# Kernel optimization log

Measured on AMD Instinct MI355X. Metric: run time of the kernel, lower is better.

Reference implementation:

```python
import jax, jax.numpy as jnp
import numpy as np

N, E, HN, K = 4096, 8192, 1024, 8
NF, EF = 128, 64
NH = [256, 256]
EH = [64, 64]
EMB = NH[-1] + len(EH)  # 258
BN_EPS = 1e-5


def setup_inputs() -> dict:
    key = jax.random.key(0)
    ks = jax.random.split(key, 16)

    def nrm(k, shape, fan):
        return jax.random.normal(k, shape, jnp.float32) / np.float32(np.sqrt(fan))

    return {
        "X_n": jax.random.normal(ks[0], (N, NF), jnp.float32),
        "X_e": jax.random.normal(ks[1], (E, EF), jnp.float32),
        # row-normalized-ish adjacency and scaled Laplacian to keep activations bounded
        "A_tilde": jax.random.uniform(ks[2], (N, N), jnp.float32) / np.float32(N),
        "L1_tilde": jax.random.normal(ks[3], (E, E), jnp.float32) / np.float32(np.sqrt(E)),
        "B1": jax.random.normal(ks[4], (N, E), jnp.float32) / np.float32(np.sqrt(E)),
        # GNN params (Linear stores weight as [out, in])
        "gnn_W1": nrm(ks[5], (NH[0], NF), NF), "gnn_b1": jnp.zeros((NH[0],), jnp.float32),
        "gnn_W2": nrm(ks[6], (NH[1], NH[0]), NH[0]), "gnn_b2": jnp.zeros((NH[1],), jnp.float32),
        # HoSC layer 1: in=EF, out=EH[0]
        "hosc_W1": nrm(ks[7], (EH[0], EF), EF), "hosc_b1": jnp.zeros((EH[0],), jnp.float32),
        "bn1_g": jnp.ones((EH[0],), jnp.float32), "bn1_b": jnp.zeros((EH[0],), jnp.float32),
        # HoSC layer 2: in=1 (after channel-max), out=EH[1]
        "hosc_W2": nrm(ks[8], (EH[1], 1), 1), "hosc_b2": jnp.zeros((EH[1],), jnp.float32),
        "bn2_g": jnp.ones((EH[1],), jnp.float32), "bn2_b": jnp.zeros((EH[1],), jnp.float32),
        # heads
        "node_W": nrm(ks[9], (1, EMB), EMB), "node_b": jnp.zeros((1,), jnp.float32),
        "edge_W": nrm(ks[10], (1, len(EH)), len(EH)), "edge_b": jnp.zeros((1,), jnp.float32),
        "hyper_W": nrm(ks[11], (1, EMB), EMB), "hyper_b": jnp.zeros((1,), jnp.float32),
        "hyperedges": jax.random.randint(ks[12], (HN, K), 0, N, jnp.int64),
    }


def _bn(x, g, b):
    # training-mode BatchNorm1d: biased batch statistics over rows
    m = jnp.mean(x, axis=0)
    v = jnp.var(x, axis=0)
    return g * (x - m) / jnp.sqrt(v + BN_EPS) + b


def _hosc_layer(Z, L1, W, bias, g, b):
    Zt = Z @ W.T + bias            # [E, out]
    Zc = L1 @ Zt                   # [E, out]
    Zp = jax.nn.relu(_bn(Zc, g, b))
    return jnp.max(Zp, axis=1, keepdims=True)  # [E, 1]


def reference(X_n, X_e, A_tilde, L1_tilde, B1,
              gnn_W1, gnn_b1, gnn_W2, gnn_b2,
              hosc_W1, hosc_b1, bn1_g, bn1_b,
              hosc_W2, hosc_b2, bn2_g, bn2_b,
              node_W, node_b, edge_W, edge_b, hyper_W, hyper_b,
              hyperedges):
    # --- GNN over nodes ---
    H = jax.nn.relu((A_tilde @ X_n) @ gnn_W1.T + gnn_b1)   # [N, 256]
    H_n = jax.nn.relu((A_tilde @ H) @ gnn_W2.T + gnn_b2)   # [N, 256]

    # --- HoSC over edges ---
    Z1 = _hosc_layer(X_e, L1_tilde, hosc_W1, hosc_b1, bn1_g, bn1_b)  # [E, 1]
    Z2 = _hosc_layer(Z1, L1_tilde, hosc_W2, hosc_b2, bn2_g, bn2_b)   # [E, 1]
    Z_H = jnp.concatenate([Z1, Z2], axis=1)                 # [E, 2]

    # --- fuse edge info into nodes ---
    H_e = B1 @ Z_H                                          # [N, 2]
    Hcat = jnp.concatenate([H_n, H_e], axis=1)              # [N, 258]

    node_prob = jax.nn.sigmoid(Hcat @ node_W.T + node_b).squeeze(-1)  # [N]
    edge_prob = jax.nn.sigmoid(Z_H @ edge_W.T + edge_b).squeeze(-1)   # [E]

    # vectorized hyperedge gather-mean-linear-sigmoid (fixed-size hyperedges)
    hfeat = Hcat[hyperedges].mean(axis=1)                   # [HN, 258]
    hyperedge_prob = jax.nn.sigmoid(hfeat @ hyper_W.T + hyper_b)  # [HN, 1]

    return node_prob, edge_prob, hyperedge_prob, Hcat
```

## Files before the change

### kernel.cpp

```cpp
#include <hip/hip_runtime.h>
#include <hip/hip_bf16.h>

using f32x4  = __attribute__((ext_vector_type(4))) float;
using u32x4  = __attribute__((ext_vector_type(4))) unsigned int;
using bf16x8 = __attribute__((ext_vector_type(8))) short;

__device__ __forceinline__ ushort f2bf(float x) {
    union { __hip_bfloat16 h; ushort u; } cv;
    cv.h = __float2bfloat16(x);
    return cv.u;
}
__device__ __forceinline__ unsigned pk2(float lo, float hi) {
    return (unsigned)f2bf(lo) | ((unsigned)f2bf(hi) << 16);
}
__device__ __forceinline__ float sigmoidf_(float x) { return 1.f / (1.f + expf(-x)); }

template<int NSUM, bool A_BF16, bool ABR, bool SPLIT, bool RELU, bool BF16_OUT, bool HAS_BIAS>
__device__ __forceinline__ void gemm_body(
    ushort* As, ushort* Bs,
    const void* __restrict__ Avoid, const ushort* __restrict__ B,
    const float* __restrict__ abias, const float* __restrict__ bias,
    float* __restrict__ Cf, ushort* __restrict__ Cb,
    int M, int N, int K, int ldc, int kPerChunk, long pStride,
    int bx, int by, int bz)
{
    const int tid  = threadIdx.x;
    const int lane = tid & 63;
    const int wid  = tid >> 6;
    const int wr   = wid >> 1, wc = wid & 1;
    const int g    = lane >> 4, lr = lane & 15;
    const long m0  = (long)bx * 128;
    const int  n0  = by * 64;

    int kbeg = 0, kend = K;
    if (SPLIT) { kbeg = bz * kPerChunk; kend = kbeg + kPerChunk; if (kend > K) kend = K; }

    const int bkr = tid & 31;
    const int bcb = tid >> 5;

    const float*  Af = (const float*)Avoid;
    const ushort* Ab = (const ushort*)Avoid;

    f32x4 pa[4];
    u32x4 pab[2];
    u32x4 pb;

    auto loadT = [&](int k0) {
        if (A_BF16) {
#pragma unroll
            for (int i = 0; i < 2; i++) {
                int s = tid + 256 * i; int row = s >> 2, c8 = s & 3;
                pab[i] = *(const u32x4*)(Ab + (m0 + row) * (long)K + k0 + c8 * 8);
            }
        } else {
#pragma unroll
            for (int i = 0; i < 4; i++) {
                int s = tid + 256 * i; int row = s >> 3, c4 = s & 7;
                const float* base = Af + (m0 + row) * (long)K + k0 + c4 * 4;
                f32x4 v = *(const f32x4*)base;
                if (NSUM > 0) {
#pragma unroll
                    for (int z = 1; z < NSUM; z++) v += *(const f32x4*)(base + z * pStride);
                }
                if (ABR) {
                    f32x4 bq = *(const f32x4*)(abias + k0 + c4 * 4);
                    v.x = fmaxf(v.x + bq.x, 0.f);
                    v.y = fmaxf(v.y + bq.y, 0.f);
                    v.z = fmaxf(v.z + bq.z, 0.f);
                    v.w = fmaxf(v.w + bq.w, 0.f);
                }
                pa[i] = v;
            }
        }
        pb = *(const u32x4*)(B + (long)(k0 + bkr) * N + n0 + bcb * 8);
    };
    auto storeT = [&]() {
        if (A_BF16) {
#pragma unroll
            for (int i = 0; i < 2; i++) {
                int s = tid + 256 * i; int row = s >> 2, c8 = s & 3;
                *(u32x4*)(&As[row * 40 + c8 * 8]) = pab[i];
            }
        } else {
#pragma unroll
            for (int i = 0; i < 4; i++) {
                int s = tid + 256 * i; int row = s >> 3, c4 = s & 7;
                ushort4 w;
                w.x = f2bf(pa[i].x); w.y = f2bf(pa[i].y);
                w.z = f2bf(pa[i].z); w.w = f2bf(pa[i].w);
                *(ushort4*)(&As[row * 40 + c4 * 4]) = w;
            }
        }
        const ushort* p8 = (const ushort*)&pb;
#pragma unroll
        for (int j = 0; j < 8; j++) Bs[(bcb * 8 + j) * 40 + bkr] = p8[j];
    };

    f32x4 acc[4][2] = {};

    const int nk = (kend - kbeg) >> 5;
    loadT(kbeg);
    for (int t = 0; t < nk; ++t) {
        storeT();
        __syncthreads();
        if (t + 1 < nk) loadT(kbeg + ((t + 1) << 5));
        bf16x8 af[4], bfr[2];
#pragma unroll
        for (int fm = 0; fm < 4; fm++)
            af[fm] = *(const bf16x8*)(&As[(wr * 64 + fm * 16 + lr) * 40 + g * 8]);
#pragma unroll
        for (int fn = 0; fn < 2; fn++)
            bfr[fn] = *(const bf16x8*)(&Bs[(wc * 32 + fn * 16 + lr) * 40 + g * 8]);
#pragma unroll
        for (int fm = 0; fm < 4; fm++)
#pragma unroll
            for (int fn = 0; fn < 2; fn++)
                acc[fm][fn] = __builtin_amdgcn_mfma_f32_16x16x32_bf16(af[fm], bfr[fn], acc[fm][fn], 0, 0, 0);
        __syncthreads();
    }

    if (SPLIT) {
        float* P = Cf + (long)bz * M * N;
#pragma unroll
        for (int fm = 0; fm < 4; fm++)
#pragma unroll
            for (int fn = 0; fn < 2; fn++)
#pragma unroll
                for (int rr = 0; rr < 4; rr++) {
                    long row = m0 + wr * 64 + fm * 16 + g * 4 + rr;
                    int  col = n0 + wc * 32 + fn * 16 + lr;
                    P[row * N + col] = acc[fm][fn][rr];
                }
    } else {
#pragma unroll
        for (int fm = 0; fm < 4; fm++)
#pragma unroll
            for (int fn = 0; fn < 2; fn++)
#pragma unroll
                for (int rr = 0; rr < 4; rr++) {
                    long row = m0 + wr * 64 + fm * 16 + g * 4 + rr;
                    int  col = n0 + wc * 32 + fn * 16 + lr;
                    float v = acc[fm][fn][rr];
                    if (HAS_BIAS) v += bias[col];
                    if (RELU) v = fmaxf(v, 0.f);
                    if (BF16_OUT) Cb[row * ldc + col] = f2bf(v);
                    else          Cf[row * ldc + col] = v;
                }
    }
}

__global__ __launch_bounds__(256)
void prep_k(const float* __restrict__ A, ushort* __restrict__ Abf,
            const float* __restrict__ Xn, const float* __restrict__ W1, ushort* __restrict__ T1,
            const float* __restrict__ Xe, const float* __restrict__ Wh,
            const float* __restrict__ hb, ushort* __restrict__ Zt1,
            const float* __restrict__ W2, ushort* __restrict__ W2t,
            float* __restrict__ stats)
{
    __shared__ float xs[1024];
    int b = blockIdx.x, t = threadIdx.x;
    if (b < 8192) {
        long j = (long)b * 256 + t;
        f32x4 v0 = ((const f32x4*)A)[2 * j];
        f32x4 v1 = ((const f32x4*)A)[2 * j + 1];
        u32x4 w;
        w.x = pk2(v0.x, v0.y); w.y = pk2(v0.z, v0.w);
        w.z = pk2(v1.x, v1.y); w.w = pk2(v1.z, v1.w);
        ((u32x4*)Abf)[j] = w;
    } else if (b < 8704) {
        int r0 = (b - 8192) * 8;
        for (int idx = t; idx < 1024; idx += 256) xs[idx] = Xn[(long)r0 * 128 + idx];
        __syncthreads();
        float acc[8] = {};
        const float* wrow = W1 + (long)t * 128;
        for (int i = 0; i < 128; i++) {
            float w = wrow[i];
#pragma unroll
            for (int r = 0; r < 8; r++) acc[r] += xs[r * 128 + i] * w;
        }
#pragma unroll
        for (int r = 0; r < 8; r++) T1[(long)(r0 + r) * 256 + t] = f2bf(acc[r]);
    } else if (b < 10752) {
        int row = (b - 8704) * 4 + (t >> 6);
        int o   = t & 63;
        const float* xr = Xe + (long)row * 64;
        const float* wr = Wh + (long)o * 64;
        float acc = hb[o];
#pragma unroll 8
        for (int i = 0; i < 64; i++) acc += xr[i] * wr[i];
        Zt1[(long)row * 64 + o] = f2bf(acc);
    } else if (b < 11008) {
        int j = (b - 10752) * 256 + t;
        int i = j >> 8, o = j & 255;
        W2t[j] = f2bf(W2[o * 256 + i]);
    } else {
        if (t < 256) stats[t] = 0.f;
    }
}

__device__ __forceinline__ void bnred_body(int b, const float* __restrict__ P,
                                           float* __restrict__ Zc,
                                           float* __restrict__ gsum, float* __restrict__ gsq)
{
    const long MN = 8192 * 64;
    int t = threadIdx.x;
    int c = t & 63, rg = t >> 6;
    float sx = 0.f, sq = 0.f;
    int base = b * 32 + rg;
#pragma unroll 4
    for (int i = 0; i < 8; i++) {
        long idx = (long)(base + 4 * i) * 64 + c;
        float x = 0.f;
#pragma unroll
        for (int z = 0; z < 8; z++) x += P[idx + z * MN];
        Zc[idx] = x;
        sx += x; sq += x * x;
    }
    __shared__ float ls[256], lq[256];
    ls[t] = sx; lq[t] = sq;
    __syncthreads();
    if (t < 64) {
        float a = ls[t] + ls[t + 64] + ls[t + 128] + ls[t + 192];
        float q = lq[t] + lq[t + 64] + lq[t + 128] + lq[t + 192];
        atomicAdd(&gsum[t], a);
        atomicAdd(&gsq[t], q);
    }
}

__device__ __forceinline__ void z1_body(int b, const float* __restrict__ Zc,
                                        const float* __restrict__ gsum, const float* __restrict__ gsq,
                                        const float* __restrict__ g, const float* __restrict__ bb,
                                        float* __restrict__ Z1)
{
    int w = threadIdx.x >> 6, lane = threadIdx.x & 63;
    int row = b * 4 + w;
    const float inv = 1.f / 8192.f;
    float m = gsum[lane] * inv;
    float v = gsq[lane] * inv - m * m;
    float x = Zc[row * 64 + lane];
    float y = fmaxf(g[lane] * (x - m) * rsqrtf(v + 1e-5f) + bb[lane], 0.f);
#pragma unroll
    for (int o = 32; o > 0; o >>= 1) y = fmaxf(y, __shfl_xor(y, o));
    if (lane == 0) Z1[row] = y;
}

__device__ __forceinline__ void pass2_body(int row, const float* __restrict__ L1,
                                           const float* __restrict__ Z1,
                                           float* __restrict__ s, float* __restrict__ r)
{
    int t = threadIdx.x;
    int l = t & 63, w = t >> 6;
    const f32x4* rp = (const f32x4*)(L1 + (long)row * 8192);
    const f32x4* z4 = (const f32x4*)Z1;
    float as = 0.f, ar = 0.f;
#pragma unroll 4
    for (int k = 0; k < 8; k++) {
        f32x4 v = rp[t + 256 * k];
        f32x4 z = z4[t + 256 * k];
        as += v.x * z.x + v.y * z.y + v.z * z.z + v.w * z.w;
        ar += v.x + v.y + v.z + v.w;
    }
#pragma unroll
    for (int o = 32; o > 0; o >>= 1) { as += __shfl_xor(as, o); ar += __shfl_xor(ar, o); }
    __shared__ float sw[4], rw[4];
    if (l == 0) { sw[w] = as; rw[w] = ar; }
    __syncthreads();
    if (t == 0) {
        s[row] = sw[0] + sw[1] + sw[2] + sw[3];
        r[row] = rw[0] + rw[1] + rw[2] + rw[3];
    }
}

__device__ __forceinline__ void hcatred_body(int b, const float* __restrict__ P2,
                                             const float* __restrict__ b2, float* __restrict__ hcat)
{
    const long MNq = (long)4096 * 256 / 4;
    int j = b * 256 + threadIdx.x;
    int row = j >> 6, c4 = (j & 63) * 4;
    const f32x4* Q = (const f32x4*)P2;
    f32x4 v = Q[j] + Q[j + MNq] + Q[j + 2 * MNq] + Q[j + 3 * MNq];
    f32x4 bq = *(const f32x4*)(b2 + c4);
    float* dst = hcat + (long)row * 258 + c4;
    float2 lo = { fmaxf(v.x + bq.x, 0.f), fmaxf(v.y + bq.y, 0.f) };
    float2 hi = { fmaxf(v.z + bq.z, 0.f), fmaxf(v.w + bq.w, 0.f) };
    *(float2*)dst = lo;
    *(float2*)(dst + 2) = hi;
}

__global__ __launch_bounds__(256)
void dual_a_k(const float* __restrict__ L1, const ushort* __restrict__ Zt1, float* __restrict__ Pa,
              const ushort* __restrict__ Abf, const ushort* __restrict__ T1, float* __restrict__ Pb)
{
    __shared__ ushort As[128 * 40];
    __shared__ ushort Bs[64 * 40];
    int bid = blockIdx.x;
    if (bid < 512) {
        gemm_body<0, false, false, true, false, false, false>(
            As, Bs, L1, Zt1, nullptr, nullptr, Pa, nullptr,
            8192, 64, 8192, 64, 1024, 0, bid & 63, 0, bid >> 6);
    } else {
        int b = bid - 512;
        gemm_body<0, true, false, true, false, false, false>(
            As, Bs, Abf, T1, nullptr, nullptr, Pb, nullptr,
            4096, 256, 4096, 256, 1024, 0, b & 31, (b >> 5) & 3, b >> 7);
    }
}

__global__ __launch_bounds__(256)
void dual_b_k(const float* __restrict__ Pb, const float* __restrict__ gb1,
              const ushort* __restrict__ W2t, ushort* __restrict__ T2,
              const float* __restrict__ Pa, float* __restrict__ Zc1,
              float* __restrict__ gsum, float* __restrict__ gsq)
{
    __shared__ ushort As[128 * 40];
    __shared__ ushort Bs[64 * 40];
    int bid = blockIdx.x;
    if (bid < 128) {
        gemm_body<4, false, true, false, false, true, false>(
            As, Bs, Pb, W2t, gb1, nullptr, nullptr, T2,
            4096, 256, 256, 256, 0, (long)4096 * 256, bid & 31, bid >> 5, 0);
    } else {
        bnred_body(bid - 128, Pa, Zc1, gsum, gsq);
    }
}

__global__ __launch_bounds__(256)
void dual_c_k(const ushort* __restrict__ Abf, const ushort* __restrict__ T2, float* __restrict__ Pa,
              const float* __restrict__ Zc1, const float* __restrict__ gsum,
              const float* __restrict__ gsq, const float* __restrict__ bn1g,
              const float* __restrict__ bn1b, float* __restrict__ Z1)
{
    __shared__ ushort As[128 * 40];
    __shared__ ushort Bs[64 * 40];
    int bid = blockIdx.x;
    if (bid < 512) {
        gemm_body<0, true, false, true, false, false, false>(
            As, Bs, Abf, T2, nullptr, nullptr, Pa, nullptr,
            4096, 256, 4096, 256, 1024, 0, bid & 31, (bid >> 5) & 3, bid >> 7);
    } else {
        z1_body(bid - 512, Zc1, gsum, gsq, bn1g, bn1b, Z1);
    }
}

__global__ __launch_bounds__(256)
void dual_d_k(const float* __restrict__ Pa, const float* __restrict__ gb2, float* __restrict__ hcat,
              const float* __restrict__ L1, const float* __restrict__ Z1,
              float* __restrict__ s, float* __restrict__ r)
{
    int bid = blockIdx.x;
    if (bid < 1024) hcatred_body(bid, Pa, gb2, hcat);
    else            pass2_body(bid - 1024, L1, Z1, s, r);
}

__global__ __launch_bounds__(1024) void stats2_k(const float* __restrict__ s, const float* __restrict__ r,
                                                 float* __restrict__ S5)
{
    int t = threadIdx.x, l = t & 63, w = t >> 6;
    float Ss = 0, Sr = 0, Sss = 0, Srr = 0, Ssr = 0;
    for (int i = t; i < 8192; i += 1024) {
        float sv = s[i], rv = r[i];
        Ss += sv; Sr += rv; Sss += sv * sv; Srr += rv * rv; Ssr += sv * rv;
    }
#pragma unroll
    for (int o = 32; o > 0; o >>= 1) {
        Ss += __shfl_xor(Ss, o); Sr += __shfl_xor(Sr, o);
        Sss += __shfl_xor(Sss, o); Srr += __shfl_xor(Srr, o); Ssr += __shfl_xor(Ssr, o);
    }
    __shared__ float buf[16][5];
    if (l == 0) { buf[w][0] = Ss; buf[w][1] = Sr; buf[w][2] = Sss; buf[w][3] = Srr; buf[w][4] = Ssr; }
    __syncthreads();
    if (t < 5) {
        float a = 0.f;
#pragma unroll
        for (int i = 0; i < 16; i++) a += buf[i][t];
        S5[t] = a;
    }
}

__global__ __launch_bounds__(256) void z2_edge_k(const float* __restrict__ s, const float* __restrict__ r,
                                                 const float* __restrict__ S,
                                                 const float* __restrict__ W2, const float* __restrict__ b2,
                                                 const float* __restrict__ g2, const float* __restrict__ bb2,
                                                 const float* __restrict__ eW, const float* __restrict__ eb,
                                                 const float* __restrict__ Z1,
                                                 float* __restrict__ Z2, float* __restrict__ edge_out)
{
    int w = threadIdx.x >> 6, lane = threadIdx.x & 63;
    int row = blockIdx.x * 4 + w;
    const float inv = 1.f / 8192.f;
    float ms = S[0] * inv, mr = S[1] * inv;
    float vs = S[2] * inv - ms * ms;
    float vr = S[3] * inv - mr * mr;
    float cv = S[4] * inv - ms * mr;
    float w2 = W2[lane], bz = b2[lane];
    float mc = w2 * ms + bz * mr;
    float vc = w2 * w2 * vs + 2.f * w2 * bz * cv + bz * bz * vr;
    float x  = w2 * s[row] + bz * r[row];
    float y  = fmaxf(g2[lane] * (x - mc) * rsqrtf(vc + 1e-5f) + bb2[lane], 0.f);
#pragma unroll
    for (int o = 32; o > 0; o >>= 1) y = fmaxf(y, __shfl_xor(y, o));
    if (lane == 0) {
        Z2[row] = y;
        float e = Z1[row] * eW[0] + y * eW[1] + eb[0];
        edge_out[row] = sigmoidf_(e);
    }
}

__global__ __launch_bounds__(256) void he_node_k(const float* __restrict__ B1, const float* __restrict__ Z1,
                                                 const float* __restrict__ Z2, float* __restrict__ hcat,
                                                 const float* __restrict__ nW, const float* __restrict__ nb,
                                                 float* __restrict__ node_out)
{
    int n = blockIdx.x, t = threadIdx.x;
    int l = t & 63, w = t >> 6;
    const f32x4* rp  = (const f32x4*)(B1 + (long)n * 8192);
    const f32x4* z1v = (const f32x4*)Z1;
    const f32x4* z2v = (const f32x4*)Z2;
    float a1 = 0.f, a2 = 0.f;
#pragma unroll 4
    for (int k = 0; k < 8; k++) {
        f32x4 v = rp[t + 256 * k];
        f32x4 p = z1v[t + 256 * k];
        f32x4 q = z2v[t + 256 * k];
        a1 += v.x * p.x + v.y * p.y + v.z * p.z + v.w * p.w;
        a2 += v.x * q.x + v.y * q.y + v.z * q.z + v.w * q.w;
    }
    float d = hcat[(long)n * 258 + t] * nW[t];
#pragma unroll
    for (int o = 32; o > 0; o >>= 1) {
        a1 += __shfl_xor(a1, o); a2 += __shfl_xor(a2, o); d += __shfl_xor(d, o);
    }
    __shared__ float s1[4], s2[4], s3[4];
    if (l == 0) { s1[w] = a1; s2[w] = a2; s3[w] = d; }
    __syncthreads();
    if (t == 0) {
        float A1 = s1[0] + s1[1] + s1[2] + s1[3];
        float A2 = s2[0] + s2[1] + s2[2] + s2[3];
        float D  = s3[0] + s3[1] + s3[2] + s3[3];
        hcat[(long)n * 258 + 256] = A1;
        hcat[(long)n * 258 + 257] = A2;
        node_out[n] = sigmoidf_(D + A1 * nW[256] + A2 * nW[257] + nb[0]);
    }
}

__global__ __launch_bounds__(256) void hyper_k(const void* __restrict__ he_idx,
                                               const float* __restrict__ hcat,
                                               const float* __restrict__ hW, const float* __restrict__ hb,
                                               float* __restrict__ out)
{
    int w = threadIdx.x >> 6, lane = threadIdx.x & 63;
    int h = blockIdx.x * 4 + w;
    const unsigned int* u = (const unsigned int*)he_idx;
    unsigned int odd = u[2 * lane + 1];
    bool is64 = __all(odd == 0u);
    float acc = 0.f;
    for (int k = 0; k < 8; k++) {
        int idx;
        if (is64) idx = (int)((const long long*)he_idx)[h * 8 + k];
        else      idx = ((const int*)he_idx)[h * 8 + k];
        const float* hr = hcat + (long)idx * 258;
        for (int d = lane; d < 258; d += 64) acc += hr[d] * hW[d];
    }
    acc *= 0.125f;
#pragma unroll
    for (int o = 32; o > 0; o >>= 1) acc += __shfl_xor(acc, o);
    if (lane == 0) out[h] = sigmoidf_(acc + hb[0]);
}

extern "C" void kernel_launch(void* const* d_in, const int* in_sizes, int n_in,
                              void* d_out, int out_size, void* d_ws, size_t ws_size,
                              hipStream_t stream)
{
    const float* X_n  = (const float*)d_in[0];
    const float* X_e  = (const float*)d_in[1];
    const float* A_t  = (const float*)d_in[2];
    const float* L1   = (const float*)d_in[3];
    const float* B1   = (const float*)d_in[4];
    const float* gW1  = (const float*)d_in[5];
    const float* gb1  = (const float*)d_in[6];
    const float* gW2  = (const float*)d_in[7];
    const float* gb2  = (const float*)d_in[8];
    const float* hW1  = (const float*)d_in[9];
    const float* hb1  = (const float*)d_in[10];
    const float* bn1g = (const float*)d_in[11];
    const float* bn1b = (const float*)d_in[12];
    const float* hW2  = (const float*)d_in[13];
    const float* hb2  = (const float*)d_in[14];
    const float* bn2g = (const float*)d_in[15];
    const float* bn2b = (const float*)d_in[16];
    const float* nW   = (const float*)d_in[17];
    const float* nb   = (const float*)d_in[18];
    const float* eW   = (const float*)d_in[19];
    const float* ebb  = (const float*)d_in[20];
    const float* yW   = (const float*)d_in[21];
    const float* yb   = (const float*)d_in[22];
    const void*  he   = d_in[23];

    float* out       = (float*)d_out;
    float* out_node  = out;
    float* out_edge  = out + 4096;
    float* out_hyper = out + 12288;
    float* hcat      = out + 13312;

    size_t off = 0;
    auto alloc = [&](size_t bytes) {
        void* p = (char*)d_ws + off;
        off = (off + bytes + 255) & ~(size_t)255;
        return p;
    };
    ushort* Abf   = (ushort*)alloc((size_t)4096 * 4096 * 2);
    ushort* T1    = (ushort*)alloc(4096 * 256 * 2);
    ushort* T2    = (ushort*)alloc(4096 * 256 * 2);
    ushort* Zt1   = (ushort*)alloc(8192 * 64 * 2);
    ushort* W2t   = (ushort*)alloc(256 * 256 * 2);
    float*  Zc1   = (float*)alloc(8192 * 64 * 4);
    float*  stats = (float*)alloc(256 * 4);
    float*  gsum  = stats;
    float*  gsq   = stats + 64;
    float*  S5    = stats + 128;
    float*  Z1    = (float*)alloc(8192 * 4);
    float*  Z2    = (float*)alloc(8192 * 4);
    float*  sbuf  = (float*)alloc(8192 * 4);
    float*  rbuf  = (float*)alloc(8192 * 4);
    float*  Pa    = (float*)alloc((size_t)8192 * 64 * 8 * 4);
    float*  Pb    = (float*)alloc((size_t)4096 * 256 * 4 * 4);

    prep_k<<<11009, 256, 0, stream>>>(A_t, Abf, X_n, gW1, T1, X_e, hW1, hb1, Zt1,
                                      gW2, W2t, stats);

    dual_a_k<<<1024, 256, 0, stream>>>(L1, Zt1, Pa, Abf, T1, Pb);

    dual_b_k<<<384, 256, 0, stream>>>(Pb, gb1, W2t, T2, Pa, Zc1, gsum, gsq);

    dual_c_k<<<2560, 256, 0, stream>>>(Abf, T2, Pa, Zc1, gsum, gsq, bn1g, bn1b, Z1);

    dual_d_k<<<9216, 256, 0, stream>>>(Pa, gb2, hcat, L1, Z1, sbuf, rbuf);

    stats2_k<<<1, 1024, 0, stream>>>(sbuf, rbuf, S5);

    z2_edge_k<<<2048, 256, 0, stream>>>(sbuf, rbuf, S5, hW2, hb2, bn2g, bn2b,
                                        eW, ebb, Z1, Z2, out_edge);

    he_node_k<<<4096, 256, 0, stream>>>(B1, Z1, Z2, hcat, nW, nb, out_node);

    hyper_k<<<256, 256, 0, stream>>>(he, hcat, yW, yb, out_hyper);
}
```

Before: 291.6 us.

## Deepen split-K partitions, replace BN atomics with last-block reduction, fold stats kernel

Raises split-K depth for the L1 GEMM from 8 to 32 chunks and for the A_tilde GEMMs from 4 to 8, so many more blocks run in the first and third stages. The reduction kernels are widened to sum the extra partials. BN1 statistics now go into per-block partial buffers and are finished by the last-arriving block through a counter, instead of atomics on shared accumulators. The separate single-block stats2 kernel is removed, and each z2_edge block recomputes the global s/r statistics itself. In exchange, much more partial-sum traffic goes through memory and every z2 block rereads the full s/r arrays.

```diff
diff --git a/kernel.cpp b/kernel.cpp
--- a/kernel.cpp
+++ b/kernel.cpp
@@ -200,30 +200,53 @@
 
 __device__ __forceinline__ void bnred_body(int b, const float* __restrict__ P,
                                            float* __restrict__ Zc,
-                                           float* __restrict__ gsum, float* __restrict__ gsq)
-{
-    const long MN = 8192 * 64;
+                                           float* __restrict__ pstats,
+                                           float* __restrict__ gsum, float* __restrict__ gsq,
+                                           unsigned* __restrict__ ctr)
+{
+    const long MNq = (long)8192 * 64 / 4;
     int t = threadIdx.x;
-    int c = t & 63, rg = t >> 6;
-    float sx = 0.f, sq = 0.f;
-    int base = b * 32 + rg;
-#pragma unroll 4
-    for (int i = 0; i < 8; i++) {
-        long idx = (long)(base + 4 * i) * 64 + c;
-        float x = 0.f;
-#pragma unroll
-        for (int z = 0; z < 8; z++) x += P[idx + z * MN];
-        Zc[idx] = x;
-        sx += x; sq += x * x;
-    }
-    __shared__ float ls[256], lq[256];
-    ls[t] = sx; lq[t] = sq;
+    f32x4 sx = {0.f, 0.f, 0.f, 0.f};
+    f32x4 sq = {0.f, 0.f, 0.f, 0.f};
+    const f32x4* Q = (const f32x4*)P;
+#pragma unroll
+    for (int it = 0; it < 2; it++) {
+        long q = (long)b * 512 + it * 256 + t;
+        f32x4 x = {0.f, 0.f, 0.f, 0.f};
+#pragma unroll 8
+        for (int z = 0; z < 32; z++) x += Q[q + z * MNq];
+        ((f32x4*)Zc)[q] = x;
+        sx += x;
+        sq.x += x.x * x.x; sq.y += x.y * x.y; sq.z += x.z * x.z; sq.w += x.w * x.w;
+    }
+    __shared__ float ls[256][8];
+#pragma unroll
+    for (int j = 0; j < 4; j++) { ls[t][j] = sx[j]; ls[t][4 + j] = sq[j]; }
     __syncthreads();
     if (t < 64) {
-        float a = ls[t] + ls[t + 64] + ls[t + 128] + ls[t + 192];
-        float q = lq[t] + lq[t + 64] + lq[t + 128] + lq[t + 192];
-        atomicAdd(&gsum[t], a);
-        atomicAdd(&gsq[t], q);
+        int cg = t >> 2, j = t & 3;
+        float a = 0.f, qq = 0.f;
+#pragma unroll
+        for (int k = 0; k < 16; k++) { a += ls[cg + 16 * k][j]; qq += ls[cg + 16 * k][4 + j]; }
+        pstats[b * 128 + t]      = a;
+        pstats[b * 128 + 64 + t] = qq;
+    }
+    __threadfence();
+    __syncthreads();
+    __shared__ unsigned lastflag;
+    if (t == 0) {
+        unsigned old = atomicAdd(ctr, 1u);
+        lastflag = (old == 255u);
+    }
+    __syncthreads();
+    if (lastflag) {
+        __threadfence();
+        if (t < 128) {
+            float a = 0.f;
+            for (int bb = 0; bb < 256; bb++) a += pstats[bb * 128 + t];
+            if (t < 64) gsum[t] = a;
+            else        gsq[t - 64] = a;
+        }
     }
 }
 
@@ -271,14 +294,16 @@
     }
 }
 
-__device__ __forceinline__ void hcatred_body(int b, const float* __restrict__ P2,
+__device__ __forceinline__ void hcatred_body(int b, const float* __restrict__ P,
                                              const float* __restrict__ b2, float* __restrict__ hcat)
 {
     const long MNq = (long)4096 * 256 / 4;
     int j = b * 256 + threadIdx.x;
     int row = j >> 6, c4 = (j & 63) * 4;
-    const f32x4* Q = (const f32x4*)P2;
-    f32x4 v = Q[j] + Q[j + MNq] + Q[j + 2 * MNq] + Q[j + 3 * MNq];
+    const f32x4* Q = (const f32x4*)P;
+    f32x4 v = {0.f, 0.f, 0.f, 0.f};
+#pragma unroll
+    for (int z = 0; z < 8; z++) v += Q[j + z * MNq];
     f32x4 bq = *(const f32x4*)(b2 + c4);
     float* dst = hcat + (long)row * 258 + c4;
     float2 lo = { fmaxf(v.x + bq.x, 0.f), fmaxf(v.y + bq.y, 0.f) };
@@ -294,15 +319,15 @@
     __shared__ ushort As[128 * 40];
     __shared__ ushort Bs[64 * 40];
     int bid = blockIdx.x;
-    if (bid < 512) {
+    if (bid < 2048) {
         gemm_body<0, false, false, true, false, false, false>(
             As, Bs, L1, Zt1, nullptr, nullptr, Pa, nullptr,
-            8192, 64, 8192, 64, 1024, 0, bid & 63, 0, bid >> 6);
+            8192, 64, 8192, 64, 256, 0, bid & 63, 0, bid >> 6);
     } else {
-        int b = bid - 512;
+        int b = bid - 2048;
         gemm_body<0, true, false, true, false, false, false>(
             As, Bs, Abf, T1, nullptr, nullptr, Pb, nullptr,
-            4096, 256, 4096, 256, 1024, 0, b & 31, (b >> 5) & 3, b >> 7);
+            4096, 256, 4096, 256, 512, 0, b & 31, (b >> 5) & 3, b >> 7);
     }
 }
 
@@ -310,22 +335,23 @@
 void dual_b_k(const float* __restrict__ Pb, const float* __restrict__ gb1,
               const ushort* __restrict__ W2t, ushort* __restrict__ T2,
               const float* __restrict__ Pa, float* __restrict__ Zc1,
-              float* __restrict__ gsum, float* __restrict__ gsq)
+              float* __restrict__ pstats,
+              float* __restrict__ gsum, float* __restrict__ gsq, unsigned* __restrict__ ctr)
 {
     __shared__ ushort As[128 * 40];
     __shared__ ushort Bs[64 * 40];
     int bid = blockIdx.x;
     if (bid < 128) {
-        gemm_body<4, false, true, false, false, true, false>(
+        gemm_body<8, false, true, false, false, true, false>(
             As, Bs, Pb, W2t, gb1, nullptr, nullptr, T2,
             4096, 256, 256, 256, 0, (long)4096 * 256, bid & 31, bid >> 5, 0);
     } else {
-        bnred_body(bid - 128, Pa, Zc1, gsum, gsq);
+        bnred_body(bid - 128, Pa, Zc1, pstats, gsum, gsq, ctr);
     }
 }
 
 __global__ __launch_bounds__(256)
-void dual_c_k(const ushort* __restrict__ Abf, const ushort* __restrict__ T2, float* __restrict__ Pa,
+void dual_c_k(const ushort* __restrict__ Abf, const ushort* __restrict__ T2, float* __restrict__ Pb,
               const float* __restrict__ Zc1, const float* __restrict__ gsum,
               const float* __restrict__ gsq, const float* __restrict__ bn1g,
               const float* __restrict__ bn1b, float* __restrict__ Z1)
@@ -333,31 +359,36 @@
     __shared__ ushort As[128 * 40];
     __shared__ ushort Bs[64 * 40];
     int bid = blockIdx.x;
-    if (bid < 512) {
+    if (bid < 1024) {
         gemm_body<0, true, false, true, false, false, false>(
-            As, Bs, Abf, T2, nullptr, nullptr, Pa, nullptr,
-            4096, 256, 4096, 256, 1024, 0, bid & 31, (bid >> 5) & 3, bid >> 7);
+            As, Bs, Abf, T2, nullptr, nullptr, Pb, nullptr,
+            4096, 256, 4096, 256, 512, 0, bid & 31, (bid >> 5) & 3, bid >> 7);
     } else {
-        z1_body(bid - 512, Zc1, gsum, gsq, bn1g, bn1b, Z1);
+        z1_body(bid - 1024, Zc1, gsum, gsq, bn1g, bn1b, Z1);
     }
 }
 
 __global__ __launch_bounds__(256)
-void dual_d_k(const float* __restrict__ Pa, const float* __restrict__ gb2, float* __restrict__ hcat,
+void dual_d_k(const float* __restrict__ Pb, const float* __restrict__ gb2, float* __restrict__ hcat,
               const float* __restrict__ L1, const float* __restrict__ Z1,
               float* __restrict__ s, float* __restrict__ r)
 {
     int bid = blockIdx.x;
-    if (bid < 1024) hcatred_body(bid, Pa, gb2, hcat);
+    if (bid < 1024) hcatred_body(bid, Pb, gb2, hcat);
     else            pass2_body(bid - 1024, L1, Z1, s, r);
 }
 
-__global__ __launch_bounds__(1024) void stats2_k(const float* __restrict__ s, const float* __restrict__ r,
-                                                 float* __restrict__ S5)
+__global__ __launch_bounds__(256)
+void z2_edge_k(const float* __restrict__ s, const float* __restrict__ r,
+               const float* __restrict__ W2, const float* __restrict__ b2,
+               const float* __restrict__ g2, const float* __restrict__ bb2,
+               const float* __restrict__ eW, const float* __restrict__ eb,
+               const float* __restrict__ Z1,
+               float* __restrict__ Z2, float* __restrict__ edge_out)
 {
     int t = threadIdx.x, l = t & 63, w = t >> 6;
     float Ss = 0, Sr = 0, Sss = 0, Srr = 0, Ssr = 0;
-    for (int i = t; i < 8192; i += 1024) {
+    for (int i = t; i < 8192; i += 256) {
         float sv = s[i], rv = r[i];
         Ss += sv; Sr += rv; Sss += sv * sv; Srr += rv * rv; Ssr += sv * rv;
     }
@@ -366,40 +397,29 @@
         Ss += __shfl_xor(Ss, o); Sr += __shfl_xor(Sr, o);
         Sss += __shfl_xor(Sss, o); Srr += __shfl_xor(Srr, o); Ssr += __shfl_xor(Ssr, o);
     }
-    __shared__ float buf[16][5];
+    __shared__ float buf[4][5];
     if (l == 0) { buf[w][0] = Ss; buf[w][1] = Sr; buf[w][2] = Sss; buf[w][3] = Srr; buf[w][4] = Ssr; }
     __syncthreads();
-    if (t < 5) {
-        float a = 0.f;
-#pragma unroll
-        for (int i = 0; i < 16; i++) a += buf[i][t];
-        S5[t] = a;
-    }
-}
-
-__global__ __launch_bounds__(256) void z2_edge_k(const float* __restrict__ s, const float* __restrict__ r,
-                                                 const float* __restrict__ S,
-                                                 const float* __restrict__ W2, const float* __restrict__ b2,
-                                                 const float* __restrict__ g2, const float* __restrict__ bb2,
-                                                 const float* __restrict__ eW, const float* __restrict__ eb,
-                                                 const float* __restrict__ Z1,
-                                                 float* __restrict__ Z2, float* __restrict__ edge_out)
-{
-    int w = threadIdx.x >> 6, lane = threadIdx.x & 63;
+    float S0 = buf[0][0] + buf[1][0] + buf[2][0] + buf[3][0];
+    float S1 = buf[0][1] + buf[1][1] + buf[2][1] + buf[3][1];
+    float S2 = buf[0][2] + buf[1][2] + buf[2][2] + buf[3][2];
+    float S3 = buf[0][3] + buf[1][3] + buf[2][3] + buf[3][3];
+    float S4 = buf[0][4] + buf[1][4] + buf[2][4] + buf[3][4];
+
     int row = blockIdx.x * 4 + w;
     const float inv = 1.f / 8192.f;
-    float ms = S[0] * inv, mr = S[1] * inv;
-    float vs = S[2] * inv - ms * ms;
-    float vr = S[3] * inv - mr * mr;
-    float cv = S[4] * inv - ms * mr;
-    float w2 = W2[lane], bz = b2[lane];
+    float ms = S0 * inv, mr = S1 * inv;
+    float vs = S2 * inv - ms * ms;
+    float vr = S3 * inv - mr * mr;
+    float cv = S4 * inv - ms * mr;
+    float w2 = W2[l], bz = b2[l];
     float mc = w2 * ms + bz * mr;
     float vc = w2 * w2 * vs + 2.f * w2 * bz * cv + bz * bz * vr;
     float x  = w2 * s[row] + bz * r[row];
-    float y  = fmaxf(g2[lane] * (x - mc) * rsqrtf(vc + 1e-5f) + bb2[lane], 0.f);
+    float y  = fmaxf(g2[l] * (x - mc) * rsqrtf(vc + 1e-5f) + bb2[l], 0.f);
 #pragma unroll
     for (int o = 32; o > 0; o >>= 1) y = fmaxf(y, __shfl_xor(y, o));
-    if (lane == 0) {
+    if (l == 0) {
         Z2[row] = y;
         float e = Z1[row] * eW[0] + y * eW[1] + eb[0];
         edge_out[row] = sigmoidf_(e);
@@ -508,37 +528,36 @@
         off = (off + bytes + 255) & ~(size_t)255;
         return p;
     };
-    ushort* Abf   = (ushort*)alloc((size_t)4096 * 4096 * 2);
-    ushort* T1    = (ushort*)alloc(4096 * 256 * 2);
-    ushort* T2    = (ushort*)alloc(4096 * 256 * 2);
-    ushort* Zt1   = (ushort*)alloc(8192 * 64 * 2);
-    ushort* W2t   = (ushort*)alloc(256 * 256 * 2);
-    float*  Zc1   = (float*)alloc(8192 * 64 * 4);
-    float*  stats = (float*)alloc(256 * 4);
-    float*  gsum  = stats;
-    float*  gsq   = stats + 64;
-    float*  S5    = stats + 128;
-    float*  Z1    = (float*)alloc(8192 * 4);
-    float*  Z2    = (float*)alloc(8192 * 4);
-    float*  sbuf  = (float*)alloc(8192 * 4);
-    float*  rbuf  = (float*)alloc(8192 * 4);
-    float*  Pa    = (float*)alloc((size_t)8192 * 64 * 8 * 4);
-    float*  Pb    = (float*)alloc((size_t)4096 * 256 * 4 * 4);
+    ushort* Abf    = (ushort*)alloc((size_t)4096 * 4096 * 2);
+    ushort* T1     = (ushort*)alloc(4096 * 256 * 2);
+    ushort* T2     = (ushort*)alloc(4096 * 256 * 2);
+    ushort* Zt1    = (ushort*)alloc(8192 * 64 * 2);
+    ushort* W2t    = (ushort*)alloc(256 * 256 * 2);
+    float*  Zc1    = (float*)alloc(8192 * 64 * 4);
+    float*  stats  = (float*)alloc(256 * 4);
+    float*  gsum   = stats;
+    float*  gsq    = stats + 64;
+    unsigned* ctr  = (unsigned*)(stats + 192);
+    float*  pstats = (float*)alloc(256 * 128 * 4);
+    float*  Z1     = (float*)alloc(8192 * 4);
+    float*  Z2     = (float*)alloc(8192 * 4);
+    float*  sbuf   = (float*)alloc(8192 * 4);
+    float*  rbuf   = (float*)alloc(8192 * 4);
+    float*  Pa     = (float*)alloc((size_t)8192 * 64 * 32 * 4);
+    float*  Pb     = (float*)alloc((size_t)4096 * 256 * 8 * 4);
 
     prep_k<<<11009, 256, 0, stream>>>(A_t, Abf, X_n, gW1, T1, X_e, hW1, hb1, Zt1,
                                       gW2, W2t, stats);
 
-    dual_a_k<<<1024, 256, 0, stream>>>(L1, Zt1, Pa, Abf, T1, Pb);
-
-    dual_b_k<<<384, 256, 0, stream>>>(Pb, gb1, W2t, T2, Pa, Zc1, gsum, gsq);
-
-    dual_c_k<<<2560, 256, 0, stream>>>(Abf, T2, Pa, Zc1, gsum, gsq, bn1g, bn1b, Z1);
-
-    dual_d_k<<<9216, 256, 0, stream>>>(Pa, gb2, hcat, L1, Z1, sbuf, rbuf);
-
-    stats2_k<<<1, 1024, 0, stream>>>(sbuf, rbuf, S5);
-
-    z2_edge_k<<<2048, 256, 0, stream>>>(sbuf, rbuf, S5, hW2, hb2, bn2g, bn2b,
+    dual_a_k<<<3072, 256, 0, stream>>>(L1, Zt1, Pa, Abf, T1, Pb);
+
+    dual_b_k<<<384, 256, 0, stream>>>(Pb, gb1, W2t, T2, Pa, Zc1, pstats, gsum, gsq, ctr);
+
+    dual_c_k<<<3072, 256, 0, stream>>>(Abf, T2, Pb, Zc1, gsum, gsq, bn1g, bn1b, Z1);
+
+    dual_d_k<<<9216, 256, 0, stream>>>(Pb, gb2, hcat, L1, Z1, sbuf, rbuf);
+
+    z2_edge_k<<<2048, 256, 0, stream>>>(sbuf, rbuf, hW2, hb2, bn2g, bn2b,
                                         eW, ebb, Z1, Z2, out_edge);
 
     he_node_k<<<4096, 256, 0, stream>>>(B1, Z1, Z2, hcat, nW, nb, out_node);
```

Measured after the change: 380.4 us. +30.5%, slower.

## Store GEMM B operands transposed to vectorize shared-memory B staging

Applied to the files above, without the earlier changes.

Changes the B operand of all GEMMs to an N-major (transposed) layout, so each thread loads 8 contiguous k values and writes them to shared memory with one 16-byte store. Previously the tile was transposed through 8 scalar LDS writes per thread. Producers are updated to match: prep writes T1 and Zt1 transposed, W2 is no longer transposed, and the T2 GEMM gains a transposed bf16 epilogue. The transposed global writes in prep (strided scalar stores for Zt1T) and the new epilogue may be less coalesced. The epilogue also has a dead ReLU line.

```diff
diff --git a/kernel.cpp b/kernel.cpp
--- a/kernel.cpp
+++ b/kernel.cpp
@@ -15,10 +15,10 @@
 }
 __device__ __forceinline__ float sigmoidf_(float x) { return 1.f / (1.f + expf(-x)); }
 
-template<int NSUM, bool A_BF16, bool ABR, bool SPLIT, bool RELU, bool BF16_OUT, bool HAS_BIAS>
+template<int NSUM, bool A_BF16, bool ABR, bool SPLIT, bool RELU, bool BF16_OUT, bool CT_OUT, bool HAS_BIAS>
 __device__ __forceinline__ void gemm_body(
     ushort* As, ushort* Bs,
-    const void* __restrict__ Avoid, const ushort* __restrict__ B,
+    const void* __restrict__ Avoid, const ushort* __restrict__ BT,
     const float* __restrict__ abias, const float* __restrict__ bias,
     float* __restrict__ Cf, ushort* __restrict__ Cb,
     int M, int N, int K, int ldc, int kPerChunk, long pStride,
@@ -35,8 +35,8 @@
     int kbeg = 0, kend = K;
     if (SPLIT) { kbeg = bz * kPerChunk; kend = kbeg + kPerChunk; if (kend > K) kend = K; }
 
-    const int bkr = tid & 31;
-    const int bcb = tid >> 5;
+    const int bn = tid >> 2;
+    const int bk = (tid & 3) * 8;
 
     const float*  Af = (const float*)Avoid;
     const ushort* Ab = (const ushort*)Avoid;
@@ -72,7 +72,7 @@
                 pa[i] = v;
             }
         }
-        pb = *(const u32x4*)(B + (long)(k0 + bkr) * N + n0 + bcb * 8);
+        pb = *(const u32x4*)(BT + (long)(n0 + bn) * K + k0 + bk);
     };
     auto storeT = [&]() {
         if (A_BF16) {
@@ -91,9 +91,7 @@
                 *(ushort4*)(&As[row * 40 + c4 * 4]) = w;
             }
         }
-        const ushort* p8 = (const ushort*)&pb;
-#pragma unroll
-        for (int j = 0; j < 8; j++) Bs[(bcb * 8 + j) * 40 + bkr] = p8[j];
+        *(u32x4*)(&Bs[bn * 40 + bk]) = pb;
     };
 
     f32x4 acc[4][2] = {};
@@ -131,6 +129,21 @@
                     int  col = n0 + wc * 32 + fn * 16 + lr;
                     P[row * N + col] = acc[fm][fn][rr];
                 }
+    } else if (CT_OUT) {
+#pragma unroll
+        for (int fm = 0; fm < 4; fm++)
+#pragma unroll
+            for (int fn = 0; fn < 2; fn++) {
+                long row0 = m0 + wr * 64 + fm * 16 + g * 4;
+                int  col  = n0 + wc * 32 + fn * 16 + lr;
+                ushort4 w;
+                w.x = f2bf(fmaxf(acc[fm][fn][0], RELU ? 0.f : acc[fm][fn][0]));
+                w.x = f2bf(acc[fm][fn][0]);
+                w.y = f2bf(acc[fm][fn][1]);
+                w.z = f2bf(acc[fm][fn][2]);
+                w.w = f2bf(acc[fm][fn][3]);
+                *(ushort4*)(Cb + (long)col * M + row0) = w;
+            }
     } else {
 #pragma unroll
         for (int fm = 0; fm < 4; fm++)
@@ -151,10 +164,10 @@
 
 __global__ __launch_bounds__(256)
 void prep_k(const float* __restrict__ A, ushort* __restrict__ Abf,
-            const float* __restrict__ Xn, const float* __restrict__ W1, ushort* __restrict__ T1,
+            const float* __restrict__ Xn, const float* __restrict__ W1, ushort* __restrict__ T1T,
             const float* __restrict__ Xe, const float* __restrict__ Wh,
-            const float* __restrict__ hb, ushort* __restrict__ Zt1,
-            const float* __restrict__ W2, ushort* __restrict__ W2t,
+            const float* __restrict__ hb, ushort* __restrict__ Zt1T,
+            const float* __restrict__ W2, ushort* __restrict__ W2b,
             float* __restrict__ stats)
 {
     __shared__ float xs[1024];
@@ -178,8 +191,10 @@
 #pragma unroll
             for (int r = 0; r < 8; r++) acc[r] += xs[r * 128 + i] * w;
         }
-#pragma unroll
-        for (int r = 0; r < 8; r++) T1[(long)(r0 + r) * 256 + t] = f2bf(acc[r]);
+        ushort w8[8];
+#pragma unroll
+        for (int r = 0; r < 8; r++) w8[r] = f2bf(acc[r]);
+        *(u32x4*)(T1T + (long)t * 4096 + r0) = *(u32x4*)w8;
     } else if (b < 10752) {
         int row = (b - 8704) * 4 + (t >> 6);
         int o   = t & 63;
@@ -188,11 +203,10 @@
         float acc = hb[o];
 #pragma unroll 8
         for (int i = 0; i < 64; i++) acc += xr[i] * wr[i];
-        Zt1[(long)row * 64 + o] = f2bf(acc);
+        Zt1T[(long)o * 8192 + row] = f2bf(acc);
     } else if (b < 11008) {
         int j = (b - 10752) * 256 + t;
-        int i = j >> 8, o = j & 255;
-        W2t[j] = f2bf(W2[o * 256 + i]);
+        W2b[j] = f2bf(W2[j]);
     } else {
         if (t < 256) stats[t] = 0.f;
     }
@@ -271,13 +285,13 @@
     }
 }
 
-__device__ __forceinline__ void hcatred_body(int b, const float* __restrict__ P2,
+__device__ __forceinline__ void hcatred_body(int b, const float* __restrict__ P,
                                              const float* __restrict__ b2, float* __restrict__ hcat)
 {
     const long MNq = (long)4096 * 256 / 4;
     int j = b * 256 + threadIdx.x;
     int row = j >> 6, c4 = (j & 63) * 4;
-    const f32x4* Q = (const f32x4*)P2;
+    const f32x4* Q = (const f32x4*)P;
     f32x4 v = Q[j] + Q[j + MNq] + Q[j + 2 * MNq] + Q[j + 3 * MNq];
     f32x4 bq = *(const f32x4*)(b2 + c4);
     float* dst = hcat + (long)row * 258 + c4;
@@ -288,27 +302,27 @@
 }
 
 __global__ __launch_bounds__(256)
-void dual_a_k(const float* __restrict__ L1, const ushort* __restrict__ Zt1, float* __restrict__ Pa,
-              const ushort* __restrict__ Abf, const ushort* __restrict__ T1, float* __restrict__ Pb)
+void dual_a_k(const float* __restrict__ L1, const ushort* __restrict__ Zt1T, float* __restrict__ Pa,
+              const ushort* __restrict__ Abf, const ushort* __restrict__ T1T, float* __restrict__ Pb)
 {
     __shared__ ushort As[128 * 40];
     __shared__ ushort Bs[64 * 40];
     int bid = blockIdx.x;
     if (bid < 512) {
-        gemm_body<0, false, false, true, false, false, false>(
-            As, Bs, L1, Zt1, nullptr, nullptr, Pa, nullptr,
+        gemm_body<0, false, false, true, false, false, false, false>(
+            As, Bs, L1, Zt1T, nullptr, nullptr, Pa, nullptr,
             8192, 64, 8192, 64, 1024, 0, bid & 63, 0, bid >> 6);
     } else {
         int b = bid - 512;
-        gemm_body<0, true, false, true, false, false, false>(
-            As, Bs, Abf, T1, nullptr, nullptr, Pb, nullptr,
+        gemm_body<0, true, false, true, false, false, false, false>(
+            As, Bs, Abf, T1T, nullptr, nullptr, Pb, nullptr,
             4096, 256, 4096, 256, 1024, 0, b & 31, (b >> 5) & 3, b >> 7);
     }
 }
 
 __global__ __launch_bounds__(256)
 void dual_b_k(const float* __restrict__ Pb, const float* __restrict__ gb1,
-              const ushort* __restrict__ W2t, ushort* __restrict__ T2,
+              const ushort* __restrict__ W2b, ushort* __restrict__ T2T,
               const float* __restrict__ Pa, float* __restrict__ Zc1,
               float* __restrict__ gsum, float* __restrict__ gsq)
 {
@@ -316,8 +330,8 @@
     __shared__ ushort Bs[64 * 40];
     int bid = blockIdx.x;
     if (bid < 128) {
-        gemm_body<4, false, true, false, false, true, false>(
-            As, Bs, Pb, W2t, gb1, nullptr, nullptr, T2,
+        gemm_body<4, false, true, false, false, true, true, false>(
+            As, Bs, Pb, W2b, gb1, nullptr, nullptr, T2T,
             4096, 256, 256, 256, 0, (long)4096 * 256, bid & 31, bid >> 5, 0);
     } else {
         bnred_body(bid - 128, Pa, Zc1, gsum, gsq);
@@ -325,7 +339,7 @@
 }
 
 __global__ __launch_bounds__(256)
-void dual_c_k(const ushort* __restrict__ Abf, const ushort* __restrict__ T2, float* __restrict__ Pa,
+void dual_c_k(const ushort* __restrict__ Abf, const ushort* __restrict__ T2T, float* __restrict__ Pa,
               const float* __restrict__ Zc1, const float* __restrict__ gsum,
               const float* __restrict__ gsq, const float* __restrict__ bn1g,
               const float* __restrict__ bn1b, float* __restrict__ Z1)
@@ -334,8 +348,8 @@
     __shared__ ushort Bs[64 * 40];
     int bid = blockIdx.x;
     if (bid < 512) {
-        gemm_body<0, true, false, true, false, false, false>(
-            As, Bs, Abf, T2, nullptr, nullptr, Pa, nullptr,
+        gemm_body<0, true, false, true, false, false, false, false>(
+            As, Bs, Abf, T2T, nullptr, nullptr, Pa, nullptr,
             4096, 256, 4096, 256, 1024, 0, bid & 31, (bid >> 5) & 3, bid >> 7);
     } else {
         z1_body(bid - 512, Zc1, gsum, gsq, bn1g, bn1b, Z1);
@@ -508,31 +522,31 @@
         off = (off + bytes + 255) & ~(size_t)255;
         return p;
     };
-    ushort* Abf   = (ushort*)alloc((size_t)4096 * 4096 * 2);
-    ushort* T1    = (ushort*)alloc(4096 * 256 * 2);
-    ushort* T2    = (ushort*)alloc(4096 * 256 * 2);
-    ushort* Zt1   = (ushort*)alloc(8192 * 64 * 2);
-    ushort* W2t   = (ushort*)alloc(256 * 256 * 2);
-    float*  Zc1   = (float*)alloc(8192 * 64 * 4);
-    float*  stats = (float*)alloc(256 * 4);
-    float*  gsum  = stats;
-    float*  gsq   = stats + 64;
-    float*  S5    = stats + 128;
-    float*  Z1    = (float*)alloc(8192 * 4);
-    float*  Z2    = (float*)alloc(8192 * 4);
-    float*  sbuf  = (float*)alloc(8192 * 4);
-    float*  rbuf  = (float*)alloc(8192 * 4);
-    float*  Pa    = (float*)alloc((size_t)8192 * 64 * 8 * 4);
-    float*  Pb    = (float*)alloc((size_t)4096 * 256 * 4 * 4);
-
-    prep_k<<<11009, 256, 0, stream>>>(A_t, Abf, X_n, gW1, T1, X_e, hW1, hb1, Zt1,
-                                      gW2, W2t, stats);
-
-    dual_a_k<<<1024, 256, 0, stream>>>(L1, Zt1, Pa, Abf, T1, Pb);
-
-    dual_b_k<<<384, 256, 0, stream>>>(Pb, gb1, W2t, T2, Pa, Zc1, gsum, gsq);
-
-    dual_c_k<<<2560, 256, 0, stream>>>(Abf, T2, Pa, Zc1, gsum, gsq, bn1g, bn1b, Z1);
+    ushort* Abf    = (ushort*)alloc((size_t)4096 * 4096 * 2);
+    ushort* T1T    = (ushort*)alloc(4096 * 256 * 2);
+    ushort* T2T    = (ushort*)alloc(4096 * 256 * 2);
+    ushort* Zt1T   = (ushort*)alloc(8192 * 64 * 2);
+    ushort* W2b    = (ushort*)alloc(256 * 256 * 2);
+    float*  Zc1    = (float*)alloc(8192 * 64 * 4);
+    float*  stats  = (float*)alloc(256 * 4);
+    float*  gsum   = stats;
+    float*  gsq    = stats + 64;
+    float*  S5     = stats + 128;
+    float*  Z1     = (float*)alloc(8192 * 4);
+    float*  Z2     = (float*)alloc(8192 * 4);
+    float*  sbuf   = (float*)alloc(8192 * 4);
+    float*  rbuf   = (float*)alloc(8192 * 4);
+    float*  Pa     = (float*)alloc((size_t)8192 * 64 * 8 * 4);
+    float*  Pb     = (float*)alloc((size_t)4096 * 256 * 4 * 4);
+
+    prep_k<<<11009, 256, 0, stream>>>(A_t, Abf, X_n, gW1, T1T, X_e, hW1, hb1, Zt1T,
+                                      gW2, W2b, stats);
+
+    dual_a_k<<<1024, 256, 0, stream>>>(L1, Zt1T, Pa, Abf, T1T, Pb);
+
+    dual_b_k<<<384, 256, 0, stream>>>(Pb, gb1, W2b, T2T, Pa, Zc1, gsum, gsq);
+
+    dual_c_k<<<2560, 256, 0, stream>>>(Abf, T2T, Pa, Zc1, gsum, gsq, bn1g, bn1b, Z1);
 
     dual_d_k<<<9216, 256, 0, stream>>>(Pa, gb2, hcat, L1, Z1, sbuf, rbuf);
 
```

After: 296.0 us. About the same (+1.5%).
